# Performance work log

Hardware: AMD Instinct MI355X
Metric: run time of the kernel (lower is better)

Reference implementation:

```python
import jax, jax.numpy as jnp
import numpy as np

N, IN_DIM, HID, HEADS = 20000, 3000, 128, 4
S_DIM, P_DIM = 32, 32
E = 320000
NEG_SLOPE = 0.2
ETA = 1e-6


def _glorot(key, shape):
    fan_in, fan_out = shape[0], shape[-1] if len(shape) > 1 else shape[0]
    lim = np.sqrt(6.0 / (fan_in + fan_out))
    return jax.random.uniform(key, shape, jnp.float32, -lim, lim)


def _gat_params(key, in_dim, out_ch, heads, concat):
    k1, k2, k3 = jax.random.split(key, 3)
    Wl = _glorot(k1, (in_dim, heads * out_ch))
    Wr = _glorot(k2, (in_dim, heads * out_ch))
    att = _glorot(k3, (heads, out_ch))
    b = jnp.zeros((heads * out_ch,) if concat else (out_ch,), jnp.float32)
    return Wl, Wr, att, b


def setup_inputs() -> dict:
    key = jax.random.key(0)
    ks = jax.random.split(key, 6)
    x = jax.random.normal(ks[0], (N, IN_DIM), jnp.float32)
    edge_index = jax.random.randint(ks[1], (2, E), 0, N, jnp.int32)
    out = {"x": x, "edge_index": edge_index}
    for name, kk, (ind, oc, h, cc) in [
        ("s1", ks[2], (IN_DIM, HID, HEADS, True)),
        ("s2", ks[3], (HID * HEADS, S_DIM * 2, 1, False)),
        ("p1", ks[4], (IN_DIM, HID, HEADS, True)),
        ("p2", ks[5], (HID * HEADS, P_DIM * 2, 1, False)),
    ]:
        Wl, Wr, att, b = _gat_params(kk, ind, oc, h, cc)
        out[f"Wl_{name}"] = Wl
        out[f"Wr_{name}"] = Wr
        out[f"att_{name}"] = att
        out[f"b_{name}"] = b
    return out


def gatv2(x, src, dst, Wl, Wr, att, b, heads, out_ch, concat):
    n = x.shape[0]
    xl = (x @ Wl).reshape(n, heads, out_ch)  # source transform
    xr = (x @ Wr).reshape(n, heads, out_ch)  # target transform
    m = xl[src]                                           # [E, H, C] messages
    e = jnp.sum(att * jax.nn.leaky_relu(m + xr[dst], NEG_SLOPE), axis=-1)  # [E, H]
    emax = jax.ops.segment_max(e, dst, num_segments=n)    # self-loops -> no empty segments
    ee = jnp.exp(e - emax[dst])
    denom = jax.ops.segment_sum(ee, dst, num_segments=n)
    alpha = ee / denom[dst]                               # segment softmax over incoming edges
    agg = jax.ops.segment_sum(m * alpha[..., None], dst, num_segments=n)  # [N, H, C]
    out = agg.reshape(n, heads * out_ch) if concat else agg.mean(axis=1)
    return out + b


def reference(x, edge_index, Wl_s1, Wr_s1, att_s1, b_s1, Wl_s2, Wr_s2, att_s2, b_s2,
              Wl_p1, Wr_p1, att_p1, b_p1, Wl_p2, Wr_p2, att_p2, b_p2):
    n = x.shape[0]
    loop = jnp.arange(n, dtype=edge_index.dtype)
    src = jnp.concatenate([edge_index[0], loop])  # add_self_loops (PyG default)
    dst = jnp.concatenate([edge_index[1], loop])
    s = jax.nn.relu(gatv2(x, src, dst, Wl_s1, Wr_s1, att_s1, b_s1, HEADS, HID, True))
    s = gatv2(s, src, dst, Wl_s2, Wr_s2, att_s2, b_s2, 1, S_DIM * 2, False)
    p = gatv2(x, src, dst, Wl_p1, Wr_p1, att_p1, b_p1, HEADS, HID, True)
    p = gatv2(p, src, dst, Wl_p2, Wr_p2, att_p2, b_p2, 1, P_DIM * 2, False)
    mu = jnp.concatenate([s[:, :S_DIM], p[:, :P_DIM]], axis=-1)
    sig = jnp.concatenate([jax.nn.softplus(s[:, S_DIM:]) + ETA,
                           jax.nn.softplus(p[:, P_DIM:]) + ETA], axis=-1)
    return mu, sig
```

## Files before the change

### kernel.cpp

```cpp
#include <hip/hip_runtime.h>
#include <cstdint>

#define NN     20000
#define NE     320000
#define ETOT   340000
#define K1R    3000
#define K1     3072
#define NPAD   20224
#define NCOL1  2048
#define LDA2   512
#define MU_SZ  1280000

typedef __bf16 bf16x8 __attribute__((ext_vector_type(8)));
typedef float f32x4 __attribute__((ext_vector_type(4)));
typedef unsigned short u16x8 __attribute__((ext_vector_type(8)));

__device__ inline unsigned short f2bf(float f) {
  union { float f; unsigned u; } v; v.f = f;
  unsigned r = v.u + 0x7FFFu + ((v.u >> 16) & 1u);
  return (unsigned short)(r >> 16);
}
__device__ inline float bf2f(unsigned short h) {
  union { unsigned u; float f; } v; v.u = ((unsigned)h) << 16;
  return v.f;
}

typedef const __attribute__((address_space(1))) void* gas1_t;
typedef __attribute__((address_space(3))) void* las3_t;
__device__ inline void llds16(const void* g, void* l) {
  __builtin_amdgcn_global_load_lds((gas1_t)(uintptr_t)g,
                                   (las3_t)(uint32_t)(uintptr_t)l, 16, 0, 0);
}

#define PB_PW1  1536
#define PB_CNT  (PB_PW1 + 1329)
#define PB_CVT  (PB_CNT + 30336)

__global__ __launch_bounds__(256)
void k_prep(const float* __restrict__ X, unsigned short* __restrict__ Xb,
            const float* __restrict__ W0, const float* __restrict__ W1,
            const float* __restrict__ W2, const float* __restrict__ W3,
            unsigned short* __restrict__ Wp,
            const int* __restrict__ ei, int* __restrict__ counts) {
  __shared__ float tile[64][65];
  int b = blockIdx.x, tid = threadIdx.x;

  if (b < PB_PW1) {
    int k0 = (b % 48) * 64, n0 = (b / 48) * 64;
    int m = n0 >> 9, c0 = n0 & 511;
    const float* W = (m == 0) ? W0 : (m == 1) ? W1 : (m == 2) ? W2 : W3;
    int tx = tid & 63, ty = tid >> 6;
#pragma unroll
    for (int rep = 0; rep < 16; rep++) {
      int i = ty + rep * 4;
      int k = k0 + i;
      tile[i][tx] = (k < K1R) ? W[(size_t)k * 512 + c0 + tx] : 0.f;
    }
    __syncthreads();
#pragma unroll
    for (int rep = 0; rep < 16; rep++) {
      int i = ty + rep * 4;
      Wp[(size_t)(n0 + i) * K1 + k0 + tx] = f2bf(tile[tx][i]);
    }
  } else if (b < PB_CNT) {
    int e = (b - PB_PW1) * 256 + tid;
    if (e < ETOT) {
      int dst = (e < NE) ? ei[NE + e] : (e - NE);
      atomicAdd(&counts[dst], 1);
    }
  } else {
    const int CH = K1 / 8;
    int idx = (b - PB_CNT) * 256 + tid;
    if (idx >= NPAD * CH) return;
    int r = idx / CH, c8 = (idx % CH) * 8;
    u16x8 o;
    if (r < NN && c8 < K1R) {
      const float4* p = (const float4*)(X + (size_t)r * K1R + c8);
      float4 a = p[0], bb = p[1];
      o[0]=f2bf(a.x); o[1]=f2bf(a.y); o[2]=f2bf(a.z); o[3]=f2bf(a.w);
      o[4]=f2bf(bb.x); o[5]=f2bf(bb.y); o[6]=f2bf(bb.z); o[7]=f2bf(bb.w);
    } else {
#pragma unroll
      for (int j = 0; j < 8; j++) o[j] = 0;
    }
    *(u16x8*)(Xb + (size_t)r * K1 + c8) = o;
  }
}


__global__ __launch_bounds__(256)
void k_pack_w2b(const float* __restrict__ Wl_s, const float* __restrict__ Wr_s,
                const float* __restrict__ Wl_p, const float* __restrict__ Wr_p,
                unsigned short* __restrict__ B2s, unsigned short* __restrict__ B2p) {
  int gidx = blockIdx.x * 256 + threadIdx.x;
  int br = gidx >> 16, idx = gidx & 65535;
  const float* Wl = br ? Wl_p : Wl_s;
  const float* Wr = br ? Wr_p : Wr_s;
  unsigned short* B2 = br ? B2p : B2s;
  int n = idx >> 9, k = idx & 511;
  float v = (n < 64) ? Wl[(size_t)k * 64 + n] : Wr[(size_t)k * 64 + (n - 64)];
  B2[idx] = f2bf(v);
}


__global__ void k_scan(const int* __restrict__ counts, int* __restrict__ row_ptr) {
  __shared__ int part[1024];
  int t = threadIdx.x;
  int base = t * 20;
  int loc[20];
  int s = 0;
#pragma unroll
  for (int i = 0; i < 20; i++) {
    int idx = base + i;
    loc[i] = s;
    s += (idx < NN) ? counts[idx] : 0;
  }
  part[t] = s;
  __syncthreads();
  for (int off = 1; off < 1024; off <<= 1) {
    int v = (t >= off) ? part[t - off] : 0;
    __syncthreads();
    part[t] += v;
    __syncthreads();
  }
  int pre = (t > 0) ? part[t - 1] : 0;
#pragma unroll
  for (int i = 0; i < 20; i++) {
    int idx = base + i;
    if (idx <= NN) row_ptr[idx] = pre + loc[i];
  }
}

__global__ __launch_bounds__(256)
void k_scatter(const int* __restrict__ ei, const int* __restrict__ row_ptr,
               int* __restrict__ counts, int* __restrict__ csr_src) {
  int e = blockIdx.x * 256 + threadIdx.x;
  if (e >= ETOT) return;
  int s_, d_;
  if (e < NE) { s_ = ei[e]; d_ = ei[NE + e]; } else { s_ = d_ = e - NE; }
  int old = atomicSub(&counts[d_], 1);
  csr_src[row_ptr[d_] + old - 1] = s_;
}


#define NT1 48

#define STAGE_ONE do { \
  if (sctr < 4 * NT1) { \
    int ts_ = sctr >> 2, u_ = sctr & 3, sb_ = ts_ & 1; \
    const unsigned short* gb_; char* lb_; int rb_; \
    if (u_ == 0)      { gb_ = A; rb_ = bmBase + 128; lb_ = lds + (sb_*2+1)*16384; } \
    else if (u_ == 1) { gb_ = B; rb_ = bnBase + 128; lb_ = lds + 65536 + (sb_*2+1)*16384; } \
    else if (u_ == 2) { gb_ = B; rb_ = bnBase;       lb_ = lds + 65536 + (sb_*2+0)*16384; } \
    else              { gb_ = A; rb_ = bmBase;       lb_ = lds + (sb_*2+0)*16384; } \
    const unsigned short* g0_ = gb_ + (size_t)(rb_ + trow) * 3072 + ts_ * 64 + scol; \
    llds16(g0_, lb_ + wid * 1024); \
    llds16(g0_ + (size_t)64 * 3072, lb_ + 8192 + wid * 1024); \
    sctr++; \
  } \
} while (0)

#define RDA(DST, BASE) do { \
  _Pragma("unroll") \
  for (int mi = 0; mi < 2; mi++) { \
    int r_ = rw * 32 + mi * 16 + l15; \
    DST[0][mi] = *(const bf16x8*)((BASE) + r_ * 128 + sw0); \
    DST[1][mi] = *(const bf16x8*)((BASE) + r_ * 128 + sw1); \
  } \
} while (0)

#define RDB(DST, BASE) do { \
  _Pragma("unroll") \
  for (int ni = 0; ni < 4; ni++) { \
    int r_ = cw * 64 + ni * 16 + l15; \
    DST[0][ni] = *(const bf16x8*)((BASE) + r_ * 128 + sw0); \
    DST[1][ni] = *(const bf16x8*)((BASE) + r_ * 128 + sw1); \
  } \
} while (0)

#define MF(MH, NH, AV, BV) do { \
  __builtin_amdgcn_s_setprio(1); \
  _Pragma("unroll") \
  for (int mi = 0; mi < 2; mi++) \
    _Pragma("unroll") \
    for (int ni = 0; ni < 4; ni++) { \
      acc[MH][NH][mi][ni] = __builtin_amdgcn_mfma_f32_16x16x32_bf16(AV[0][mi], BV[0][ni], acc[MH][NH][mi][ni], 0, 0, 0); \
      acc[MH][NH][mi][ni] = __builtin_amdgcn_mfma_f32_16x16x32_bf16(AV[1][mi], BV[1][ni], acc[MH][NH][mi][ni], 0, 0, 0); \
    } \
  __builtin_amdgcn_s_setprio(0); \
} while (0)

__global__ __launch_bounds__(512, 2)
void gemm256(const unsigned short* __restrict__ A, const unsigned short* __restrict__ B,
             unsigned short* __restrict__ C) {
  __shared__ char lds[131072];
  int tid = threadIdx.x, wid = tid >> 6, lane = tid & 63;
  int l15 = lane & 15;
  int rw = wid & 3, cw = wid >> 2;
  int role = (wid >> 2) & 1;
  int bid = blockIdx.x;
  int bn = bid & 7, bm = bid >> 3;
  int bmBase = bm * 256, bnBase = bn * 256;
  int trow = tid >> 3;
  int scol = ((tid & 7) ^ ((tid >> 3) & 7)) * 8;
  int sw0 = (((lane >> 4) + 0) ^ (lane & 7)) * 16;
  int sw1 = (((lane >> 4) + 4) ^ (lane & 7)) * 16;
  f32x4 acc[2][2][2][4] = {};

  int sctr = 0;
  for (int i = 0; i < 4; i++) STAGE_ONE;
  asm volatile("s_waitcnt vmcnt(0)" ::: "memory");
  __builtin_amdgcn_s_barrier();
  asm volatile("" ::: "memory");

  for (int t = 0; t < NT1; t++) {
    int buf = t & 1;
    const char* A0h = lds + (buf * 2 + 0) * 16384;
    const char* A1h = lds + (buf * 2 + 1) * 16384;
    const char* B0h = lds + 65536 + (buf * 2 + 0) * 16384;
    const char* B1h = lds + 65536 + (buf * 2 + 1) * 16384;
    bf16x8 a0[2][2], a1[2][2], b0[2][4], b1[2][4];

    if (role == 0) {
      STAGE_ONE;
      RDA(a0, A0h); RDB(b0, B0h);
      MF(0, 0, a0, b0);
      STAGE_ONE;
      RDA(a1, A1h);
      MF(1, 0, a1, b0);
      STAGE_ONE;
      RDB(b1, B1h);
      MF(1, 1, a1, b1);
      STAGE_ONE;
      MF(0, 1, a0, b1);
    } else {
      STAGE_ONE;
      RDA(a1, A1h); RDB(b1, B1h);
      MF(1, 1, a1, b1);
      STAGE_ONE;
      RDA(a0, A0h);
      MF(0, 1, a0, b1);
      STAGE_ONE;
      RDB(b0, B0h);
      MF(0, 0, a0, b0);
      STAGE_ONE;
      MF(1, 0, a1, b0);
    }
    asm volatile("s_waitcnt vmcnt(0)" ::: "memory");
    __builtin_amdgcn_s_barrier();
    asm volatile("" ::: "memory");
  }

  unsigned short (*sq)[128] = (unsigned short (*)[128])lds;
#pragma unroll
  for (int mh = 0; mh < 2; mh++)
#pragma unroll
    for (int nh = 0; nh < 2; nh++) {
      __syncthreads();
#pragma unroll
      for (int mi = 0; mi < 2; mi++)
#pragma unroll
        for (int ni = 0; ni < 4; ni++)
#pragma unroll
          for (int r = 0; r < 4; r++)
            sq[rw * 32 + mi * 16 + (lane >> 4) * 4 + r][cw * 64 + ni * 16 + l15] =
                f2bf(acc[mh][nh][mi][ni][r]);
      __syncthreads();
#pragma unroll
      for (int it = 0; it < 4; it++) {
        int idx = it * 512 + tid;
        int row = idx >> 4, ch = idx & 15;
        *(u16x8*)(C + (size_t)(bmBase + mh * 128 + row) * NCOL1 + bnBase + nh * 128 + ch * 8) =
            *(const u16x8*)&sq[row][ch * 8];
      }
    }
}


__global__ __launch_bounds__(256)
void gemm_l2(const unsigned short* __restrict__ As, const unsigned short* __restrict__ Bs,
             float* __restrict__ Cs,
             const unsigned short* __restrict__ Ap, const unsigned short* __restrict__ Bp,
             float* __restrict__ Cp) {
  const int K = LDA2, lda = LDA2, ldb = LDA2, ldc = 128, mreal = NN;
  const unsigned short* A = blockIdx.y ? Ap : As;
  const unsigned short* B = blockIdx.y ? Bp : Bs;
  float* C = blockIdx.y ? Cp : Cs;
  __shared__ char smem_raw[16384];
  unsigned short* sA = (unsigned short*)smem_raw;
  unsigned short* sB = sA + 128 * 32;
  int bm = blockIdx.x;
  int tid = threadIdx.x, wid = tid >> 6, lane = tid & 63;
  int wr = wid >> 1, wc = wid & 1;
  f32x4 acc[4][4] = {};

  int ar = 32 * wid + (lane >> 2);
  int acol = (lane & 3) * 8;
  const unsigned short* Ag = A + (size_t)(bm * 128 + ar) * lda + acol;
  const unsigned short* Bg = B + (size_t)ar * ldb + acol;
  unsigned short* la0 = sA + (wid * 2) * 512;
  unsigned short* lb0 = sB + (wid * 2) * 512;
  int frow = lane & 15, koff = (lane >> 4) * 8;

  for (int kt = 0; kt < K; kt += 32) {
    llds16(Ag + kt, la0);
    llds16(Ag + kt + (size_t)16 * lda, la0 + 512);
    llds16(Bg + kt, lb0);
    llds16(Bg + kt + (size_t)16 * ldb, lb0 + 512);
    __syncthreads();
    bf16x8 af[4], bfr[4];
#pragma unroll
    for (int mi = 0; mi < 4; mi++)
      af[mi] = *(const bf16x8*)(sA + (wr * 64 + mi * 16 + frow) * 32 + koff);
#pragma unroll
    for (int ni = 0; ni < 4; ni++)
      bfr[ni] = *(const bf16x8*)(sB + (wc * 64 + ni * 16 + frow) * 32 + koff);
#pragma unroll
    for (int mi = 0; mi < 4; mi++)
#pragma unroll
      for (int ni = 0; ni < 4; ni++)
        acc[mi][ni] = __builtin_amdgcn_mfma_f32_16x16x32_bf16(af[mi], bfr[ni], acc[mi][ni], 0, 0, 0);
    __syncthreads();
  }

#pragma unroll
  for (int mi = 0; mi < 4; mi++) {
    int grow0 = bm * 128 + wr * 64 + mi * 16 + (lane >> 4) * 4;
#pragma unroll
    for (int ni = 0; ni < 4; ni++) {
      int gcol = wc * 64 + ni * 16 + (lane & 15);
#pragma unroll
      for (int r = 0; r < 4; r++) {
        int grow = grow0 + r;
        if (grow < mreal) C[(size_t)grow * ldc + gcol] = acc[mi][ni][r];
      }
    }
  }
}


__global__ __launch_bounds__(256)
void edge_agg1(const unsigned short* __restrict__ XL1,
               const int* __restrict__ row_ptr, const int* __restrict__ csr_src,
               const float* __restrict__ att_s, const float* __restrict__ att_p,
               const float* __restrict__ b_s, const float* __restrict__ b_p,
               unsigned short* __restrict__ A2s, unsigned short* __restrict__ A2p) {
  int n = (blockIdx.x * 256 + threadIdx.x) >> 6;
  if (n >= NN) return;
  int lane = threadIdx.x & 63;
  int cb = lane * 8;
  float xs[8], xp[8], as_[8], ap_[8], aggs[8], aggp[8];
  {
    bf16x8 xsv = *(const bf16x8*)(XL1 + (size_t)n * NCOL1 + 512 + cb);
    bf16x8 xpv = *(const bf16x8*)(XL1 + (size_t)n * NCOL1 + 1536 + cb);
    float4 a0 = *(const float4*)(att_s + cb), a1 = *(const float4*)(att_s + cb + 4);
    float4 a2 = *(const float4*)(att_p + cb), a3 = *(const float4*)(att_p + cb + 4);
    as_[0]=a0.x; as_[1]=a0.y; as_[2]=a0.z; as_[3]=a0.w; as_[4]=a1.x; as_[5]=a1.y; as_[6]=a1.z; as_[7]=a1.w;
    ap_[0]=a2.x; ap_[1]=a2.y; ap_[2]=a2.z; ap_[3]=a2.w; ap_[4]=a3.x; ap_[5]=a3.y; ap_[6]=a3.z; ap_[7]=a3.w;
#pragma unroll
    for (int j = 0; j < 8; j++) { xs[j] = (float)xsv[j]; xp[j] = (float)xpv[j]; aggs[j] = 0.f; aggp[j] = 0.f; }
  }
  float Ms = -1e30f, Ss = 0.f, Mp = -1e30f, Sp = 0.f;
  int p0 = row_ptr[n], pe = row_ptr[n + 1];
  int deg = pe - p0;

  auto gS = [&](int s) { return *(const bf16x8*)(XL1 + (size_t)s * NCOL1 + cb); };
  auto gP = [&](int s) { return *(const bf16x8*)(XL1 + (size_t)s * NCOL1 + 1024 + cb); };
  auto compute = [&](bf16x8 cs, bf16x8 cp) {
    float mjs[8], mjp[8], ps_ = 0.f, pp_ = 0.f;
#pragma unroll
    for (int j = 0; j < 8; j++) {
      mjs[j] = (float)cs[j];
      float t = mjs[j] + xs[j];
      t = (t > 0.f) ? t : 0.2f * t;
      ps_ = fmaf(as_[j], t, ps_);
      mjp[j] = (float)cp[j];
      float u = mjp[j] + xp[j];
      u = (u > 0.f) ? u : 0.2f * u;
      pp_ = fmaf(ap_[j], u, pp_);
    }
#pragma unroll
    for (int w = 1; w < 16; w <<= 1) { ps_ += __shfl_xor(ps_, w); pp_ += __shfl_xor(pp_, w); }
    float nms = fmaxf(Ms, ps_);
    float fs = __expf(Ms - nms), ws_ = __expf(ps_ - nms);
    Ss = Ss * fs + ws_;
    float nmp = fmaxf(Mp, pp_);
    float fp = __expf(Mp - nmp), wp_ = __expf(pp_ - nmp);
    Sp = Sp * fp + wp_;
#pragma unroll
    for (int j = 0; j < 8; j++) {
      aggs[j] = aggs[j] * fs + ws_ * mjs[j];
      aggp[j] = aggp[j] * fp + wp_ * mjp[j];
    }
    Ms = nms; Mp = nmp;
  };

  bf16x8 s0s, s0p, s1s, s1p;
  {
    int i0 = csr_src[p0];
    s0s = gS(i0); s0p = gP(i0);
    if (deg > 1) { int i1 = csr_src[p0 + 1]; s1s = gS(i1); s1p = gP(i1); }
  }
  int p = p0;
  for (; p + 3 < pe; p += 2) {
    int ia = csr_src[p + 2], ib = csr_src[p + 3];
    bf16x8 n0s = gS(ia), n0p = gP(ia);
    bf16x8 n1s = gS(ib), n1p = gP(ib);
    compute(s0s, s0p);
    compute(s1s, s1p);
    s0s = n0s; s0p = n0p; s1s = n1s; s1p = n1p;
  }
  int r = pe - p;
  if (r == 3) {
    int i = csr_src[p + 2];
    bf16x8 ts = gS(i), tp = gP(i);
    compute(s0s, s0p); compute(s1s, s1p); compute(ts, tp);
  } else if (r == 2) {
    compute(s0s, s0p); compute(s1s, s1p);
  } else {
    compute(s0s, s0p);
  }

  float invs = 1.f / Ss, invp = 1.f / Sp;
  u16x8 hs, hp;
#pragma unroll
  for (int j = 0; j < 8; j++) {
    float v = fmaxf(aggs[j] * invs + b_s[cb + j], 0.f);
    hs[j] = f2bf(v);
    float u = aggp[j] * invp + b_p[cb + j];
    hp[j] = f2bf(u);
  }
  *(u16x8*)(A2s + (size_t)n * LDA2 + cb) = hs;
  *(u16x8*)(A2p + (size_t)n * LDA2 + cb) = hp;
}


__global__ __launch_bounds__(256)
void edge_agg2(const float* __restrict__ C2s, const float* __restrict__ C2p,
               const int* __restrict__ row_ptr, const int* __restrict__ csr_src,
               const float* __restrict__ att_s, const float* __restrict__ att_p,
               const float* __restrict__ b_s, const float* __restrict__ b_p,
               float* __restrict__ out) {
  int n = (blockIdx.x * 256 + threadIdx.x) >> 6;
  if (n >= NN) return;
  int lane = threadIdx.x & 63;
  float xrs = C2s[(size_t)n * 128 + 64 + lane];
  float xrp = C2p[(size_t)n * 128 + 64 + lane];
  float ats = att_s[lane], atp = att_p[lane];
  float Ms = -1e30f, Ss = 0.f, ags = 0.f;
  float Mp = -1e30f, Sp = 0.f, agp = 0.f;
  int p0 = row_ptr[n], pe = row_ptr[n + 1];
  int deg = pe - p0;

  auto compute = [&](float cs, float cp) {
    float t = cs + xrs; t = (t > 0.f) ? t : 0.2f * t;
    float u = cp + xrp; u = (u > 0.f) ? u : 0.2f * u;
    float ps_ = ats * t, pp_ = atp * u;
#pragma unroll
    for (int w = 1; w < 64; w <<= 1) { ps_ += __shfl_xor(ps_, w); pp_ += __shfl_xor(pp_, w); }
    float nms = fmaxf(Ms, ps_);
    float fs = __expf(Ms - nms), ws_ = __expf(ps_ - nms);
    Ss = Ss * fs + ws_; ags = ags * fs + ws_ * cs; Ms = nms;
    float nmp = fmaxf(Mp, pp_);
    float fp = __expf(Mp - nmp), wp_ = __expf(pp_ - nmp);
    Sp = Sp * fp + wp_; agp = agp * fp + wp_ * cp; Mp = nmp;
  };

  float s0c, s0d, s1c, s1d;
  {
    int i0 = csr_src[p0];
    s0c = C2s[(size_t)i0 * 128 + lane]; s0d = C2p[(size_t)i0 * 128 + lane];
    if (deg > 1) { int i1 = csr_src[p0 + 1]; s1c = C2s[(size_t)i1 * 128 + lane]; s1d = C2p[(size_t)i1 * 128 + lane]; }
  }
  int p = p0;
  for (; p + 3 < pe; p += 2) {
    int ia = csr_src[p + 2], ib = csr_src[p + 3];
    float n0c = C2s[(size_t)ia * 128 + lane], n0d = C2p[(size_t)ia * 128 + lane];
    float n1c = C2s[(size_t)ib * 128 + lane], n1d = C2p[(size_t)ib * 128 + lane];
    compute(s0c, s0d);
    compute(s1c, s1d);
    s0c = n0c; s0d = n0d; s1c = n1c; s1d = n1d;
  }
  int r = pe - p;
  if (r == 3) {
    int i = csr_src[p + 2];
    float tc = C2s[(size_t)i * 128 + lane], td = C2p[(size_t)i * 128 + lane];
    compute(s0c, s0d); compute(s1c, s1d); compute(tc, td);
  } else if (r == 2) {
    compute(s0c, s0d); compute(s1c, s1d);
  } else {
    compute(s0c, s0d);
  }

  float vs = ags / Ss + b_s[lane];
  float vp = agp / Sp + b_p[lane];
  if (lane < 32) {
    out[(size_t)n * 64 + lane] = vs;
    out[(size_t)n * 64 + 32 + lane] = vp;
  } else {
    float sps = fmaxf(vs, 0.f) + log1pf(__expf(-fabsf(vs))) + 1e-6f;
    float spp = fmaxf(vp, 0.f) + log1pf(__expf(-fabsf(vp))) + 1e-6f;
    out[(size_t)MU_SZ + n * 64 + (lane - 32)] = sps;
    out[(size_t)MU_SZ + n * 64 + 32 + (lane - 32)] = spp;
  }
}


extern "C" void kernel_launch(void* const* d_in, const int* in_sizes, int n_in,
                              void* d_out, int out_size, void* d_ws, size_t ws_size,
                              hipStream_t stream) {
  const float* x      = (const float*)d_in[0];
  const int*   ei     = (const int*)d_in[1];
  const float* Wl_s1  = (const float*)d_in[2];
  const float* Wr_s1  = (const float*)d_in[3];
  const float* att_s1 = (const float*)d_in[4];
  const float* b_s1   = (const float*)d_in[5];
  const float* Wl_s2  = (const float*)d_in[6];
  const float* Wr_s2  = (const float*)d_in[7];
  const float* att_s2 = (const float*)d_in[8];
  const float* b_s2   = (const float*)d_in[9];
  const float* Wl_p1  = (const float*)d_in[10];
  const float* Wr_p1  = (const float*)d_in[11];
  const float* att_p1 = (const float*)d_in[12];
  const float* b_p1   = (const float*)d_in[13];
  const float* Wl_p2  = (const float*)d_in[14];
  const float* Wr_p2  = (const float*)d_in[15];
  const float* att_p2 = (const float*)d_in[16];
  const float* b_p2   = (const float*)d_in[17];

  char* ws = (char*)d_ws;
  unsigned short* Xb   = (unsigned short*)(ws + 0);
  unsigned short* A2s  = (unsigned short*)(ws + 0);
  unsigned short* A2p  = (unsigned short*)(ws + 20578304);
  float*          C2s  = (float*)(ws + 41156608);
  float*          C2p  = (float*)(ws + 51396608);
  unsigned short* B2s  = (unsigned short*)(ws + 61636608);
  unsigned short* B2p  = (unsigned short*)(ws + 61767680);
  unsigned short* Wp   = (unsigned short*)(ws + 124256256);
  unsigned short* XL1  = (unsigned short*)(ws + 136839168);
  int* counts  = (int*)(ws + 219676672);
  int* row_ptr = (int*)(ws + 219836672);
  int* csr_src = (int*)(ws + 219916688);

  hipMemsetAsync(counts, 0, NN * sizeof(int), stream);

  k_prep<<<PB_CVT, 256, 0, stream>>>(x, Xb, Wl_s1, Wr_s1, Wl_p1, Wr_p1, Wp, ei, counts);
  k_scan<<<1, 1024, 0, stream>>>(counts, row_ptr);
  k_scatter<<<(ETOT + 255) / 256, 256, 0, stream>>>(ei, row_ptr, counts, csr_src);

  gemm256<<<632, 512, 0, stream>>>(Xb, Wp, XL1);

  k_pack_w2b<<<512, 256, 0, stream>>>(Wl_s2, Wr_s2, Wl_p2, Wr_p2, B2s, B2p);

  edge_agg1<<<5000, 256, 0, stream>>>(XL1, row_ptr, csr_src, att_s1, att_p1, b_s1, b_p1, A2s, A2p);

  gemm_l2<<<dim3(157, 2), 256, 0, stream>>>(A2s, B2s, C2s, A2p, B2p, C2p);

  edge_agg2<<<5000, 256, 0, stream>>>(C2s, C2p, row_ptr, csr_src, att_s2, att_p2, b_s2, b_p2, (float*)d_out);
}
```

Baseline: 575.1 us.

## Fold CSR scan into GEMM grid and merge scatter with weight packing

The single-block prefix scan becomes an extra block of the layer-1 GEMM launch, so it runs alongside the matmul instead of as its own serial launch. The edge scatter and the layer-2 weight packing are merged into one kernel, removing two launches in total. The weight arguments to k_prep are reordered, which changes the column layout of XL1, and edge_agg1's offsets are updated to match. This cuts launch gaps and the idle time of a one-block kernel, at the cost of an extra GEMM block that uses the LDS as scan scratch.

After: 555.3 us. 1.04x faster.

```diff
diff --git a/kernel.cpp b/kernel.cpp
--- a/kernel.cpp
+++ b/kernel.cpp
@@ -88,58 +88,33 @@
 }
 
 
+#define POST_SCT 1329
+#define POST_TOT (POST_SCT + 512)
+
 __global__ __launch_bounds__(256)
-void k_pack_w2b(const float* __restrict__ Wl_s, const float* __restrict__ Wr_s,
-                const float* __restrict__ Wl_p, const float* __restrict__ Wr_p,
-                unsigned short* __restrict__ B2s, unsigned short* __restrict__ B2p) {
-  int gidx = blockIdx.x * 256 + threadIdx.x;
-  int br = gidx >> 16, idx = gidx & 65535;
-  const float* Wl = br ? Wl_p : Wl_s;
-  const float* Wr = br ? Wr_p : Wr_s;
-  unsigned short* B2 = br ? B2p : B2s;
-  int n = idx >> 9, k = idx & 511;
-  float v = (n < 64) ? Wl[(size_t)k * 64 + n] : Wr[(size_t)k * 64 + (n - 64)];
-  B2[idx] = f2bf(v);
-}
-
-
-__global__ void k_scan(const int* __restrict__ counts, int* __restrict__ row_ptr) {
-  __shared__ int part[1024];
-  int t = threadIdx.x;
-  int base = t * 20;
-  int loc[20];
-  int s = 0;
-#pragma unroll
-  for (int i = 0; i < 20; i++) {
-    int idx = base + i;
-    loc[i] = s;
-    s += (idx < NN) ? counts[idx] : 0;
-  }
-  part[t] = s;
-  __syncthreads();
-  for (int off = 1; off < 1024; off <<= 1) {
-    int v = (t >= off) ? part[t - off] : 0;
-    __syncthreads();
-    part[t] += v;
-    __syncthreads();
-  }
-  int pre = (t > 0) ? part[t - 1] : 0;
-#pragma unroll
-  for (int i = 0; i < 20; i++) {
-    int idx = base + i;
-    if (idx <= NN) row_ptr[idx] = pre + loc[i];
-  }
-}
-
-__global__ __launch_bounds__(256)
-void k_scatter(const int* __restrict__ ei, const int* __restrict__ row_ptr,
-               int* __restrict__ counts, int* __restrict__ csr_src) {
-  int e = blockIdx.x * 256 + threadIdx.x;
-  if (e >= ETOT) return;
-  int s_, d_;
-  if (e < NE) { s_ = ei[e]; d_ = ei[NE + e]; } else { s_ = d_ = e - NE; }
-  int old = atomicSub(&counts[d_], 1);
-  csr_src[row_ptr[d_] + old - 1] = s_;
+void k_post(const int* __restrict__ ei, const int* __restrict__ row_ptr,
+            int* __restrict__ counts, int* __restrict__ csr_src,
+            const float* __restrict__ Wl_s2, const float* __restrict__ Wr_s2,
+            const float* __restrict__ Wl_p2, const float* __restrict__ Wr_p2,
+            unsigned short* __restrict__ B2s, unsigned short* __restrict__ B2p) {
+  int b = blockIdx.x, tid = threadIdx.x;
+  if (b < POST_SCT) {
+    int e = b * 256 + tid;
+    if (e >= ETOT) return;
+    int s_, d_;
+    if (e < NE) { s_ = ei[e]; d_ = ei[NE + e]; } else { s_ = d_ = e - NE; }
+    int old = atomicSub(&counts[d_], 1);
+    csr_src[row_ptr[d_] + old - 1] = s_;
+  } else {
+    int gidx = (b - POST_SCT) * 256 + tid;
+    int br = gidx >> 16, idx = gidx & 65535;
+    const float* Wl = br ? Wl_p2 : Wl_s2;
+    const float* Wr = br ? Wr_p2 : Wr_s2;
+    unsigned short* B2 = br ? B2p : B2s;
+    int n = idx >> 9, k = idx & 511;
+    float v = (n < 64) ? Wl[(size_t)k * 64 + n] : Wr[(size_t)k * 64 + (n - 64)];
+    B2[idx] = f2bf(v);
+  }
 }
 
 
@@ -192,9 +167,39 @@
 
 __global__ __launch_bounds__(512, 2)
 void gemm256(const unsigned short* __restrict__ A, const unsigned short* __restrict__ B,
-             unsigned short* __restrict__ C) {
+             unsigned short* __restrict__ C,
+             const int* __restrict__ counts, int* __restrict__ row_ptr) {
   __shared__ char lds[131072];
   int tid = threadIdx.x, wid = tid >> 6, lane = tid & 63;
+
+  if (blockIdx.x == 632) {
+    int* part = (int*)lds;
+    int base = tid * 40;
+    int loc[40];
+    int s = 0;
+#pragma unroll
+    for (int i = 0; i < 40; i++) {
+      int idx = base + i;
+      loc[i] = s;
+      s += (idx < NN) ? counts[idx] : 0;
+    }
+    part[tid] = s;
+    __syncthreads();
+    for (int off = 1; off < 512; off <<= 1) {
+      int v = (tid >= off) ? part[tid - off] : 0;
+      __syncthreads();
+      part[tid] += v;
+      __syncthreads();
+    }
+    int pre = (tid > 0) ? part[tid - 1] : 0;
+#pragma unroll
+    for (int i = 0; i < 40; i++) {
+      int idx = base + i;
+      if (idx <= NN) row_ptr[idx] = pre + loc[i];
+    }
+    return;
+  }
+
   int l15 = lane & 15;
   int rw = wid & 3, cw = wid >> 2;
   int role = (wid >> 2) & 1;
@@ -351,7 +356,7 @@
   int cb = lane * 8;
   float xs[8], xp[8], as_[8], ap_[8], aggs[8], aggp[8];
   {
-    bf16x8 xsv = *(const bf16x8*)(XL1 + (size_t)n * NCOL1 + 512 + cb);
+    bf16x8 xsv = *(const bf16x8*)(XL1 + (size_t)n * NCOL1 + 1024 + cb);
     bf16x8 xpv = *(const bf16x8*)(XL1 + (size_t)n * NCOL1 + 1536 + cb);
     float4 a0 = *(const float4*)(att_s + cb), a1 = *(const float4*)(att_s + cb + 4);
     float4 a2 = *(const float4*)(att_p + cb), a3 = *(const float4*)(att_p + cb + 4);
@@ -365,7 +370,7 @@
   int deg = pe - p0;
 
   auto gS = [&](int s) { return *(const bf16x8*)(XL1 + (size_t)s * NCOL1 + cb); };
-  auto gP = [&](int s) { return *(const bf16x8*)(XL1 + (size_t)s * NCOL1 + 1024 + cb); };
+  auto gP = [&](int s) { return *(const bf16x8*)(XL1 + (size_t)s * NCOL1 + 512 + cb); };
   auto compute = [&](bf16x8 cs, bf16x8 cp) {
     float mjs[8], mjp[8], ps_ = 0.f, pp_ = 0.f;
 #pragma unroll
@@ -544,13 +549,12 @@
 
   hipMemsetAsync(counts, 0, NN * sizeof(int), stream);
 
-  k_prep<<<PB_CVT, 256, 0, stream>>>(x, Xb, Wl_s1, Wr_s1, Wl_p1, Wr_p1, Wp, ei, counts);
-  k_scan<<<1, 1024, 0, stream>>>(counts, row_ptr);
-  k_scatter<<<(ETOT + 255) / 256, 256, 0, stream>>>(ei, row_ptr, counts, csr_src);
-
-  gemm256<<<632, 512, 0, stream>>>(Xb, Wp, XL1);
-
-  k_pack_w2b<<<512, 256, 0, stream>>>(Wl_s2, Wr_s2, Wl_p2, Wr_p2, B2s, B2p);
+  k_prep<<<PB_CVT, 256, 0, stream>>>(x, Xb, Wl_s1, Wl_p1, Wr_s1, Wr_p1, Wp, ei, counts);
+
+  gemm256<<<633, 512, 0, stream>>>(Xb, Wp, XL1, counts, row_ptr);
+
+  k_post<<<POST_TOT, 256, 0, stream>>>(ei, row_ptr, counts, csr_src,
+                                       Wl_s2, Wr_s2, Wl_p2, Wr_p2, B2s, B2p);
 
   edge_agg1<<<5000, 256, 0, stream>>>(XL1, row_ptr, csr_src, att_s1, att_p1, b_s1, b_p1, A2s, A2p);
 
```
